# Kernel tuning notes

Hardware: AMD Instinct MI355X
Metric: run time of the kernel (lower is better)

Reference implementation:

```python
import jax, jax.numpy as jnp
import numpy as np


def _interp_ac(x, out_hw):
    """Bilinear resize with align_corners=True; x: (B, C, H, W)."""
    def axis_interp(x, out, axis):
        n = x.shape[axis]
        pos = jnp.linspace(0.0, float(n - 1), out, dtype=x.dtype)
        i0 = jnp.floor(pos).astype(jnp.int32)
        i1 = jnp.minimum(i0 + 1, n - 1)
        w = pos - i0.astype(x.dtype)
        shp = [1] * x.ndim
        shp[axis] = out
        w = w.reshape(shp)
        return jnp.take(x, i0, axis=axis) * (1.0 - w) + jnp.take(x, i1, axis=axis) * w
    x = axis_interp(x, out_hw[0], 2)
    x = axis_interp(x, out_hw[1], 3)
    return x


def _bn(x, gamma, beta, mean, var):
    # eval-mode BatchNorm2d, eps=1e-5; x: (B, C, H, W)
    inv = jax.lax.rsqrt(var + 1e-5)
    return (x - mean[None, :, None, None]) * (gamma * inv)[None, :, None, None] + beta[None, :, None, None]


def setup_inputs() -> dict:
    key = jax.random.key(0)
    ks = jax.random.split(key, 4)
    B, C_low, H_low, W_low = 8, 64, 256, 256
    C_high, H_high, W_high = 128, 64, 64
    rdm = 64
    return {
        "x_low": jax.random.normal(ks[0], (B, C_low, H_low, W_low), jnp.float32),
        "x_high": jax.random.normal(ks[1], (B, C_high, H_high, W_high), jnp.float32),
        "red_w": jax.random.normal(ks[2], (rdm, C_high), jnp.float32) * 0.05,
        "red_gamma": jnp.ones((rdm,), jnp.float32),
        "red_beta": jnp.zeros((rdm,), jnp.float32),
        "red_mean": jnp.zeros((rdm,), jnp.float32),
        "red_var": jnp.ones((rdm,), jnp.float32),
        "cconv_w": jax.random.normal(ks[3], (rdm, 2 * rdm), jnp.float32) * 0.05,
        "cconv_b": jnp.zeros((rdm,), jnp.float32),
        "cc_gamma": jnp.ones((rdm,), jnp.float32),
        "cc_beta": jnp.zeros((rdm,), jnp.float32),
        "cc_mean": jnp.zeros((rdm,), jnp.float32),
        "cc_var": jnp.ones((rdm,), jnp.float32),
    }


def reference(x_low, x_high, red_w, red_gamma, red_beta, red_mean, red_var,
              cconv_w, cconv_b, cc_gamma, cc_beta, cc_mean, cc_var):
    B, Cl, Hl, Wl = x_low.shape
    _, Ch, Hh, Wh = x_high.shape
    N = Hh * Wh
    xh_sg = jax.lax.stop_gradient(x_high)  # torch uses x_high.detach() everywhere

    # --- cosine channel-attention branch ---
    xl = _interp_ac(x_low, (Hh, Wh)).reshape(B, Cl, N)   # (B, Cl, N)
    xh = xh_sg.reshape(B, Ch, N)                          # (B, Ch, N)
    nl = jnp.sqrt(jnp.sum(xl * xl, axis=2, keepdims=True)) + 1e-12  # (B, Cl, 1)
    nh = jnp.sqrt(jnp.sum(xh * xh, axis=2, keepdims=True)) + 1e-12  # (B, Ch, 1)
    cos = jnp.einsum('bcn,bdn->bcd', xl / nl, xh / nh)    # (B, Cl, Ch)
    cos = jax.nn.softmax(cos, axis=2)
    x_high_cos = jnp.einsum('bcd,bdn->bcn', cos, xh).reshape(B, Cl, Hh, Wh)
    x_high_cos = _interp_ac(x_high_cos, (Hl, Wl))         # (B, Cl, Hl, Wl)

    # --- reduced high-level branch (1x1 conv + BN + ReLU) ---
    red = jnp.einsum('oc,bchw->bohw', red_w, xh_sg)
    red = jax.nn.relu(_bn(red, red_gamma, red_beta, red_mean, red_var))
    red = _interp_ac(red, (Hl, Wl))                       # (B, rdm, Hl, Wl)

    # --- channel gate: adaptive avg pool -> 1x1 conv -> BN -> sigmoid ---
    pooled = jnp.mean(jnp.concatenate([x_low, red], axis=1), axis=(2, 3))  # (B, 2*rdm)
    att = pooled @ cconv_w.T + cconv_b                    # (B, rdm)
    att = jax.nn.sigmoid(_bn(att[:, :, None, None], cc_gamma, cc_beta, cc_mean, cc_var))
    red = red * att

    # --- sigmoid diffs + ReLU ---
    sl = jax.nn.sigmoid(x_low)
    diff = jnp.concatenate([sl - jax.nn.sigmoid(x_high_cos),
                            sl - jax.nn.sigmoid(red)], axis=1)
    return jax.nn.relu(diff)
```

## Files before the change

### kernel.cpp

```cpp
#include <hip/hip_runtime.h>
#include <math.h>

#define NPIX 4096
#define NLOW 65536
#define NRSTAGE 19

__device__ __forceinline__ float sigmoidf_(float x){
  return __builtin_amdgcn_rcpf(1.0f + __expf(-x));
}

__device__ __forceinline__ float wave_sum(float v){
  #pragma unroll
  for(int o=32;o;o>>=1) v += __shfl_down(v, o, 64);
  return v;
}

__global__ __launch_bounds__(512) void k_down(const float* __restrict__ xlow,
    float* __restrict__ xl, float* __restrict__ ssql, float* __restrict__ sum_low){
  __shared__ float rows[17*256];
  __shared__ float sd[16];
  int bc = blockIdx.x;
  const float4* X4 = (const float4*)(xlow + (size_t)bc*NLOW);
  float4* R4 = (float4*)rows;
  const float D = 255.0f/63.0f;
  float sum = 0.f, ssq = 0.f;
  int rt = threadIdx.x >> 6, j = threadIdx.x & 63;

  for(int it=0; it<16; ++it){
    int base = 16*it;
    __syncthreads();
    for(int i=threadIdx.x; i<1024; i+=512){
      float4 v = X4[base*64 + i];
      R4[i] = v;
      sum += (v.x+v.y)+(v.z+v.w);
    }
    if(threadIdx.x < 64){
      int srow = base+16; if(srow > 255) srow = 255;
      R4[1024 + threadIdx.x] = X4[srow*64 + threadIdx.x];
    }
    __syncthreads();
    int i0 = (int)ceilf((float)base / D);
    int i = i0 + rt;
    if(i < 64){
      float ph = i*D; int h0 = (int)ph; if(h0 > 255) h0 = 255;
      if((h0 >> 4) == it){
        float fh = ph - (float)h0;
        int h1 = h0+1; if(h1 > 255) h1 = 255;
        int hl = h0 - base, hl2 = h1 - base;
        float pw = j*D; int w0 = (int)pw; if(w0 > 255) w0 = 255;
        float fw = pw - (float)w0;
        int w1 = w0+1; if(w1 > 255) w1 = 255;
        const float* r0 = rows + hl*256; const float* r1 = rows + hl2*256;
        float v = (1.f-fh)*((1.f-fw)*r0[w0] + fw*r0[w1])
                +      fh *((1.f-fw)*r1[w0] + fw*r1[w1]);
        xl[(size_t)bc*NPIX + i*64 + j] = v;
        ssq += v*v;
      }
    }
  }
  float wa = wave_sum(sum), wb = wave_sum(ssq);
  int w = threadIdx.x >> 6;
  if((threadIdx.x & 63) == 0){ sd[w] = wa; sd[8+w] = wb; }
  __syncthreads();
  if(threadIdx.x == 0){
    float a = 0.f, b2 = 0.f;
    #pragma unroll
    for(int k=0;k<8;k++){ a += sd[k]; b2 += sd[8+k]; }
    sum_low[bc] = a;
    ssql[bc]    = b2;
  }
}

__global__ __launch_bounds__(256) void k_ssqh(const float* __restrict__ xh, float* __restrict__ ssqh){
  __shared__ float sd[4];
  int bd = blockIdx.x;
  const float4* P = (const float4*)(xh + (size_t)bd*NPIX);
  float s = 0.f;
  for(int i=threadIdx.x; i<NPIX/4; i+=256){
    float4 v = P[i];
    s += v.x*v.x + v.y*v.y + v.z*v.z + v.w*v.w;
  }
  float w = wave_sum(s);
  if((threadIdx.x & 63) == 0) sd[threadIdx.x >> 6] = w;
  __syncthreads();
  if(threadIdx.x == 0) ssqh[bd] = sd[0]+sd[1]+sd[2]+sd[3];
}

__global__ __launch_bounds__(256) void k_cospart(const float* __restrict__ xl,
                                                 const float* __restrict__ xh,
                                                 float* __restrict__ cospart){
  __shared__ float xls[64*65];
  __shared__ float xhs[128*65];
  int b = blockIdx.x >> 6;
  int chk = blockIdx.x & 63;
  int n0 = chk * 64;
  for(int idx = threadIdx.x; idx < 64*64; idx += 256){
    int c = idx >> 6, k = idx & 63;
    xls[c*65 + k] = xl[((size_t)b*64 + c)*NPIX + n0 + k];
  }
  for(int idx = threadIdx.x; idx < 128*64; idx += 256){
    int d = idx >> 6, k = idx & 63;
    xhs[d*65 + k] = xh[((size_t)b*128 + d)*NPIX + n0 + k];
  }
  __syncthreads();
  int ci = threadIdx.x & 15, di = threadIdx.x >> 4;
  int c0 = ci*4, d0 = di*8;
  float acc[4][8];
  #pragma unroll
  for(int i=0;i<4;i++)
    #pragma unroll
    for(int j=0;j<8;j++) acc[i][j] = 0.f;
  for(int k=0;k<64;k++){
    float a0 = xls[(c0+0)*65 + k];
    float a1 = xls[(c0+1)*65 + k];
    float a2 = xls[(c0+2)*65 + k];
    float a3 = xls[(c0+3)*65 + k];
    #pragma unroll
    for(int j=0;j<8;j++){
      float bv = xhs[(d0+j)*65 + k];
      acc[0][j] += a0*bv; acc[1][j] += a1*bv; acc[2][j] += a2*bv; acc[3][j] += a3*bv;
    }
  }
  float* op = cospart + (size_t)(b*64 + chk)*8192;
  #pragma unroll
  for(int i=0;i<4;i++){
    float4 v0 = make_float4(acc[i][0],acc[i][1],acc[i][2],acc[i][3]);
    float4 v1 = make_float4(acc[i][4],acc[i][5],acc[i][6],acc[i][7]);
    float4* dst = (float4*)(op + (c0+i)*128 + d0);
    dst[0] = v0; dst[1] = v1;
  }
}

__global__ __launch_bounds__(128) void k_softmax(const float* __restrict__ cospart,
    const float* __restrict__ ssql, const float* __restrict__ ssqh, float* __restrict__ p){
  int b = blockIdx.x >> 6, c = blockIdx.x & 63;
  int d = threadIdx.x;
  float s = 0.f;
  for(int chk=0; chk<64; chk++)
    s += cospart[(size_t)(b*64 + chk)*8192 + c*128 + d];
  float nl = sqrtf(ssql[b*64 + c]) + 1e-12f;
  float nh = sqrtf(ssqh[b*128 + d]) + 1e-12f;
  float cosv = s / (nl * nh);
  __shared__ float sm[2], ssum[2];
  float m = cosv;
  #pragma unroll
  for(int o=32;o;o>>=1) m = fmaxf(m, __shfl_xor(m, o, 64));
  if((threadIdx.x & 63) == 0) sm[threadIdx.x >> 6] = m;
  __syncthreads();
  m = fmaxf(sm[0], sm[1]);
  float e = __expf(cosv - m);
  float t = e;
  #pragma unroll
  for(int o=32;o;o>>=1) t += __shfl_xor(t, o, 64);
  if((threadIdx.x & 63) == 0) ssum[threadIdx.x >> 6] = t;
  __syncthreads();
  t = ssum[0] + ssum[1];
  p[(size_t)(b*64 + c)*128 + d] = e * __builtin_amdgcn_rcpf(t);
}

__global__ __launch_bounds__(256) void k_pv(const float* __restrict__ p, const float* __restrict__ red_w,
    const float* __restrict__ xh,
    const float* __restrict__ rg, const float* __restrict__ rb,
    const float* __restrict__ rm, const float* __restrict__ rv,
    float* __restrict__ xhc, float* __restrict__ red64){
  __shared__ float P_s[128*65];
  int b = blockIdx.x >> 6, chk = blockIdx.x & 63;
  int n0 = chk * 64;
  int ni = threadIdx.x & 7, ri = threadIdx.x >> 3;
  int r0 = 4*ri;
  float acc[4][8];
  #pragma unroll
  for(int i=0;i<4;i++)
    #pragma unroll
    for(int j=0;j<8;j++) acc[i][j] = 0.f;
  const float* xrow = xh + (size_t)b*128*NPIX + n0 + 8*ni;
  for(int half=0; half<2; ++half){
    int kb = half*64;
    __syncthreads();
    for(int idx = threadIdx.x; idx < 128*64; idx += 256){
      int r = idx >> 6, kk = idx & 63;
      int k = kb + kk;
      P_s[r*65 + kk] = (r < 64) ? p[((size_t)b*64 + r)*128 + k]
                                : red_w[(size_t)(r-64)*128 + k];
    }
    __syncthreads();
    #pragma unroll 4
    for(int kk=0; kk<64; ++kk){
      int k = kb + kk;
      float4 x0 = *(const float4*)(xrow + (size_t)k*NPIX);
      float4 x1 = *(const float4*)(xrow + (size_t)k*NPIX + 4);
      #pragma unroll
      for(int rr=0; rr<4; rr++){
        float pw = P_s[(r0+rr)*65 + kk];
        acc[rr][0] += pw*x0.x; acc[rr][1] += pw*x0.y; acc[rr][2] += pw*x0.z; acc[rr][3] += pw*x0.w;
        acc[rr][4] += pw*x1.x; acc[rr][5] += pw*x1.y; acc[rr][6] += pw*x1.z; acc[rr][7] += pw*x1.w;
      }
    }
  }
  #pragma unroll
  for(int rr=0; rr<4; rr++){
    int r = r0 + rr;
    if(r < 64){
      float* dst = xhc + ((size_t)b*64 + r)*NPIX + n0 + 8*ni;
      *(float4*)dst     = make_float4(acc[rr][0],acc[rr][1],acc[rr][2],acc[rr][3]);
      *(float4*)(dst+4) = make_float4(acc[rr][4],acc[rr][5],acc[rr][6],acc[rr][7]);
    } else {
      int o = r - 64;
      float sc = rg[o] * rsqrtf(rv[o] + 1e-5f);
      float bs = rb[o] - rm[o]*sc;
      float* dst = red64 + ((size_t)b*64 + o)*NPIX + n0 + 8*ni;
      *(float4*)dst     = make_float4(fmaxf(fmaf(acc[rr][0],sc,bs),0.f), fmaxf(fmaf(acc[rr][1],sc,bs),0.f),
                                      fmaxf(fmaf(acc[rr][2],sc,bs),0.f), fmaxf(fmaf(acc[rr][3],sc,bs),0.f));
      *(float4*)(dst+4) = make_float4(fmaxf(fmaf(acc[rr][4],sc,bs),0.f), fmaxf(fmaf(acc[rr][5],sc,bs),0.f),
                                      fmaxf(fmaf(acc[rr][6],sc,bs),0.f), fmaxf(fmaf(acc[rr][7],sc,bs),0.f));
    }
  }
}

__global__ __launch_bounds__(256) void k_redmean(const float* __restrict__ red64, float* __restrict__ redmean){
  __shared__ float wv[64];
  __shared__ float sd[4];
  int bo = blockIdx.x;
  if(threadIdx.x < 64){
    int i = threadIdx.x;
    const float U = 63.0f/255.0f;
    float acc = 0.f;
    for(int k=0;k<256;k++){
      float pos = k*U;
      int i0 = (int)pos; if(i0>63) i0=63;
      float f = pos - (float)i0;
      int i1 = i0+1; if(i1>63) i1=63;
      if(i0==i) acc += 1.0f - f;
      if(i1==i) acc += f;
    }
    wv[i] = acc;
  }
  __syncthreads();
  const float* R = red64 + (size_t)bo*NPIX;
  float acc = 0.f;
  for(int t=threadIdx.x; t<NPIX; t+=256){
    int i = t>>6, j = t&63;
    acc += wv[i]*wv[j]*R[t];
  }
  float w = wave_sum(acc);
  if((threadIdx.x & 63) == 0) sd[threadIdx.x >> 6] = w;
  __syncthreads();
  if(threadIdx.x == 0) redmean[bo] = (sd[0]+sd[1]+sd[2]+sd[3]) * (1.0f/65536.0f);
}

__global__ __launch_bounds__(256) void k_final(const float* __restrict__ xlow,
    const float* __restrict__ xhc, const float* __restrict__ red64,
    const float* __restrict__ sum_low, const float* __restrict__ redmean,
    const float* __restrict__ cw, const float* __restrict__ cb,
    const float* __restrict__ g, const float* __restrict__ be,
    const float* __restrict__ mu, const float* __restrict__ va,
    float* __restrict__ out){
  __shared__ float sx[NRSTAGE*64];
  __shared__ float sr[NRSTAGE*64];
  __shared__ float s_red[2];
  __shared__ float s_att;
  int bc = blockIdx.x >> 2;
  int sl_ = blockIdx.x & 3;
  int b = bc >> 6, c = bc & 63;
  int h_start = sl_ * 64;
  const float U = 63.0f/255.0f;
  int r_lo = (int)(h_start*U);
  {
    const float* Ax = xhc   + (size_t)bc*NPIX;
    const float* Ar = red64 + (size_t)bc*NPIX;
    for(int i=threadIdx.x; i<NRSTAGE*16; i+=256){
      int row = i>>4, c4 = i&15;
      int srow = r_lo + row; if(srow > 63) srow = 63;
      ((float4*)sx)[i] = *(const float4*)(Ax + srow*64 + c4*4);
      ((float4*)sr)[i] = *(const float4*)(Ar + srow*64 + c4*4);
    }
  }
  if(threadIdx.x < 128){
    int j = threadIdx.x;
    float pj = (j < 64) ? sum_low[b*64 + j]*(1.0f/65536.0f) : redmean[b*64 + (j-64)];
    float t = cw[c*128 + j] * pj;
    float w = wave_sum(t);
    if((j & 63) == 0) s_red[j >> 6] = w;
  }
  __syncthreads();
  if(threadIdx.x == 0){
    float acc = s_red[0] + s_red[1] + cb[c];
    float sc = g[c] * rsqrtf(va[c] + 1e-5f);
    s_att = sigmoidf_((acc - mu[c])*sc + be[c]);
  }
  __syncthreads();
  float a = s_att;

  int ct = threadIdx.x & 63;
  int rt = threadIdx.x >> 6;
  float fw_[4]; bool dw_[4];
  int c0;
  {
    float pw0 = (4*ct)*U; c0 = (int)pw0; if(c0 > 63) c0 = 63;
    #pragma unroll
    for(int i=0;i<4;i++){
      int w = 4*ct + i;
      float pw = w*U;
      int w0 = (int)pw; if(w0 > 63) w0 = 63;
      fw_[i] = pw - (float)w0;
      dw_[i] = (w0 > c0);
    }
  }
  const float* XL = xlow + (size_t)bc*NLOW;
  float* O1 = out + ((size_t)(b*128) + c)*NLOW;
  float* O2 = O1 + (size_t)64*NLOW;

  #pragma unroll
  for(int it=0; it<4; ++it){
    int hbase = h_start + (it*4 + rt)*4;
    int r0 = (int)(hbase*U);
    float ax[3][3], ar[3][3];
    #pragma unroll
    for(int rr=0; rr<3; rr++){
      int rcl = r0 + rr; if(rcl > 63) rcl = 63;
      int rb_ = (rcl - r_lo)*64;
      #pragma unroll
      for(int cc=0; cc<3; cc++){
        int ccl = c0 + cc; if(ccl > 63) ccl = 63;
        ax[rr][cc] = sx[rb_ + ccl];
        ar[rr][cc] = sr[rb_ + ccl];
      }
    }
    float tx[3][4], tr_[3][4];
    #pragma unroll
    for(int rr=0; rr<3; rr++){
      #pragma unroll
      for(int i=0;i<4;i++){
        float lx0 = dw_[i] ? ax[rr][1] : ax[rr][0];
        float lx1 = dw_[i] ? ax[rr][2] : ax[rr][1];
        tx[rr][i] = lx0 + fw_[i]*(lx1 - lx0);
        float lr0 = dw_[i] ? ar[rr][1] : ar[rr][0];
        float lr1 = dw_[i] ? ar[rr][2] : ar[rr][1];
        tr_[rr][i] = lr0 + fw_[i]*(lr1 - lr0);
      }
    }
    #pragma unroll
    for(int hh=0; hh<4; ++hh){
      int h = hbase + hh;
      float ph = h*U;
      int h0 = (int)ph; if(h0 > 63) h0 = 63;
      float fh = ph - (float)h0;
      bool e = (h0 > r0);
      float4 xv = *(const float4*)(XL + h*256 + ct*4);
      float xvv[4] = {xv.x, xv.y, xv.z, xv.w};
      float o1[4], o2[4];
      #pragma unroll
      for(int i=0;i<4;i++){
        float ax0 = e ? tx[1][i] : tx[0][i];
        float ax1 = e ? tx[2][i] : tx[1][i];
        float vx = ax0 + fh*(ax1 - ax0);
        float ar0 = e ? tr_[1][i] : tr_[0][i];
        float ar1 = e ? tr_[2][i] : tr_[1][i];
        float vr = ar0 + fh*(ar1 - ar0);
        float sl = sigmoidf_(xvv[i]);
        o1[i] = fmaxf(sl - sigmoidf_(vx), 0.f);
        o2[i] = fmaxf(sl - sigmoidf_(vr*a), 0.f);
      }
      *(float4*)(O1 + h*256 + ct*4) = make_float4(o1[0],o1[1],o1[2],o1[3]);
      *(float4*)(O2 + h*256 + ct*4) = make_float4(o2[0],o2[1],o2[2],o2[3]);
    }
  }
}

extern "C" void kernel_launch(void* const* d_in, const int* in_sizes, int n_in,
                              void* d_out, int out_size, void* d_ws, size_t ws_size,
                              hipStream_t stream) {
  const float* x_low   = (const float*)d_in[0];
  const float* x_high  = (const float*)d_in[1];
  const float* red_w   = (const float*)d_in[2];
  const float* red_g   = (const float*)d_in[3];
  const float* red_b   = (const float*)d_in[4];
  const float* red_m   = (const float*)d_in[5];
  const float* red_v   = (const float*)d_in[6];
  const float* cconv_w = (const float*)d_in[7];
  const float* cconv_b = (const float*)d_in[8];
  const float* cc_g    = (const float*)d_in[9];
  const float* cc_b    = (const float*)d_in[10];
  const float* cc_m    = (const float*)d_in[11];
  const float* cc_v    = (const float*)d_in[12];
  float* out = (float*)d_out;
  float* ws  = (float*)d_ws;

  float* bufA    = ws;
  float* bufB    = ws + 2097152;
  float* p       = ws + 6291456;
  float* sum_low = ws + 6356992;
  float* ssql    = ws + 6357504;
  float* ssqh    = ws + 6358016;
  float* redmean = ws + 6359040;

  hipLaunchKernelGGL(k_down,    dim3(512),  dim3(512), 0, stream, x_low, bufA, ssql, sum_low);
  hipLaunchKernelGGL(k_ssqh,    dim3(1024), dim3(256), 0, stream, x_high, ssqh);
  hipLaunchKernelGGL(k_cospart, dim3(512),  dim3(256), 0, stream, bufA, x_high, bufB);
  hipLaunchKernelGGL(k_softmax, dim3(512),  dim3(128), 0, stream, bufB, ssql, ssqh, p);
  hipLaunchKernelGGL(k_pv,      dim3(512),  dim3(256), 0, stream, p, red_w, x_high,
                     red_g, red_b, red_m, red_v, bufB, bufA);
  hipLaunchKernelGGL(k_redmean, dim3(512),  dim3(256), 0, stream, bufA, redmean);
  hipLaunchKernelGGL(k_final,   dim3(2048), dim3(256), 0, stream, x_low, bufB, bufA,
                     sum_low, redmean, cconv_w, cconv_b, cc_g, cc_b, cc_m, cc_v, out);
}
```

Baseline: 187.1 us.

## Merge ssqh into downsample kernel, split rows, fold redmean into pv

Merges the x_high sum-of-squares kernel into the downsample kernel as extra blocks, and splits each downsample channel across two blocks to double parallelism, with partial sums combined by consumers. Computes the weighted mean of the reduced branch inside k_pv epilogue via per-chunk partials, removing the separate k_redmean kernel and its re-read of red64. This cuts two launches and one pass over a 2M-float buffer, at the cost of extra partial-sum reads in softmax and k_final.

```diff
diff --git a/kernel.cpp b/kernel.cpp
--- a/kernel.cpp
+++ b/kernel.cpp
@@ -15,18 +15,39 @@
   return v;
 }
 
-__global__ __launch_bounds__(512) void k_down(const float* __restrict__ xlow,
-    float* __restrict__ xl, float* __restrict__ ssql, float* __restrict__ sum_low){
+__global__ __launch_bounds__(512) void k_pre(const float* __restrict__ xlow,
+    const float* __restrict__ xh,
+    float* __restrict__ xl, float* __restrict__ ssql2, float* __restrict__ sum_low2,
+    float* __restrict__ ssqh){
   __shared__ float rows[17*256];
   __shared__ float sd[16];
-  int bc = blockIdx.x;
+  int bid = blockIdx.x;
+  if(bid >= 1024){
+    int s = bid - 1024;
+    int h = threadIdx.x >> 8, tid = threadIdx.x & 255;
+    int bd = 2*s + h;
+    const float4* P = (const float4*)(xh + (size_t)bd*NPIX);
+    float acc = 0.f;
+    #pragma unroll
+    for(int i=tid; i<1024; i+=256){
+      float4 v = P[i];
+      acc += v.x*v.x + v.y*v.y + v.z*v.z + v.w*v.w;
+    }
+    float w = wave_sum(acc);
+    if((threadIdx.x & 63) == 0) sd[threadIdx.x >> 6] = w;
+    __syncthreads();
+    if(tid == 0) ssqh[bd] = sd[h*4+0]+sd[h*4+1]+sd[h*4+2]+sd[h*4+3];
+    return;
+  }
+  int bc = bid >> 1, half = bid & 1;
   const float4* X4 = (const float4*)(xlow + (size_t)bc*NLOW);
   float4* R4 = (float4*)rows;
   const float D = 255.0f/63.0f;
   float sum = 0.f, ssq = 0.f;
   int rt = threadIdx.x >> 6, j = threadIdx.x & 63;
 
-  for(int it=0; it<16; ++it){
+  for(int w=0; w<8; ++w){
+    int it = half*8 + w;
     int base = 16*it;
     __syncthreads();
     for(int i=threadIdx.x; i<1024; i+=512){
@@ -59,31 +80,16 @@
     }
   }
   float wa = wave_sum(sum), wb = wave_sum(ssq);
-  int w = threadIdx.x >> 6;
-  if((threadIdx.x & 63) == 0){ sd[w] = wa; sd[8+w] = wb; }
+  int wi = threadIdx.x >> 6;
+  if((threadIdx.x & 63) == 0){ sd[wi] = wa; sd[8+wi] = wb; }
   __syncthreads();
   if(threadIdx.x == 0){
     float a = 0.f, b2 = 0.f;
     #pragma unroll
     for(int k=0;k<8;k++){ a += sd[k]; b2 += sd[8+k]; }
-    sum_low[bc] = a;
-    ssql[bc]    = b2;
-  }
-}
-
-__global__ __launch_bounds__(256) void k_ssqh(const float* __restrict__ xh, float* __restrict__ ssqh){
-  __shared__ float sd[4];
-  int bd = blockIdx.x;
-  const float4* P = (const float4*)(xh + (size_t)bd*NPIX);
-  float s = 0.f;
-  for(int i=threadIdx.x; i<NPIX/4; i+=256){
-    float4 v = P[i];
-    s += v.x*v.x + v.y*v.y + v.z*v.z + v.w*v.w;
-  }
-  float w = wave_sum(s);
-  if((threadIdx.x & 63) == 0) sd[threadIdx.x >> 6] = w;
-  __syncthreads();
-  if(threadIdx.x == 0) ssqh[bd] = sd[0]+sd[1]+sd[2]+sd[3];
+    sum_low2[bc*2 + half] = a;
+    ssql2[bc*2 + half]    = b2;
+  }
 }
 
 __global__ __launch_bounds__(256) void k_cospart(const float* __restrict__ xl,
@@ -132,13 +138,13 @@
 }
 
 __global__ __launch_bounds__(128) void k_softmax(const float* __restrict__ cospart,
-    const float* __restrict__ ssql, const float* __restrict__ ssqh, float* __restrict__ p){
+    const float* __restrict__ ssql2, const float* __restrict__ ssqh, float* __restrict__ p){
   int b = blockIdx.x >> 6, c = blockIdx.x & 63;
   int d = threadIdx.x;
   float s = 0.f;
   for(int chk=0; chk<64; chk++)
     s += cospart[(size_t)(b*64 + chk)*8192 + c*128 + d];
-  float nl = sqrtf(ssql[b*64 + c]) + 1e-12f;
+  float nl = sqrtf(ssql2[(b*64 + c)*2] + ssql2[(b*64 + c)*2 + 1]) + 1e-12f;
   float nh = sqrtf(ssqh[b*128 + d]) + 1e-12f;
   float cosv = s / (nl * nh);
   __shared__ float sm[2], ssum[2];
@@ -162,65 +168,13 @@
     const float* __restrict__ xh,
     const float* __restrict__ rg, const float* __restrict__ rb,
     const float* __restrict__ rm, const float* __restrict__ rv,
-    float* __restrict__ xhc, float* __restrict__ red64){
+    float* __restrict__ xhc, float* __restrict__ red64, float* __restrict__ part_buf){
   __shared__ float P_s[128*65];
+  __shared__ float wvv[64];
   int b = blockIdx.x >> 6, chk = blockIdx.x & 63;
   int n0 = chk * 64;
   int ni = threadIdx.x & 7, ri = threadIdx.x >> 3;
   int r0 = 4*ri;
-  float acc[4][8];
-  #pragma unroll
-  for(int i=0;i<4;i++)
-    #pragma unroll
-    for(int j=0;j<8;j++) acc[i][j] = 0.f;
-  const float* xrow = xh + (size_t)b*128*NPIX + n0 + 8*ni;
-  for(int half=0; half<2; ++half){
-    int kb = half*64;
-    __syncthreads();
-    for(int idx = threadIdx.x; idx < 128*64; idx += 256){
-      int r = idx >> 6, kk = idx & 63;
-      int k = kb + kk;
-      P_s[r*65 + kk] = (r < 64) ? p[((size_t)b*64 + r)*128 + k]
-                                : red_w[(size_t)(r-64)*128 + k];
-    }
-    __syncthreads();
-    #pragma unroll 4
-    for(int kk=0; kk<64; ++kk){
-      int k = kb + kk;
-      float4 x0 = *(const float4*)(xrow + (size_t)k*NPIX);
-      float4 x1 = *(const float4*)(xrow + (size_t)k*NPIX + 4);
-      #pragma unroll
-      for(int rr=0; rr<4; rr++){
-        float pw = P_s[(r0+rr)*65 + kk];
-        acc[rr][0] += pw*x0.x; acc[rr][1] += pw*x0.y; acc[rr][2] += pw*x0.z; acc[rr][3] += pw*x0.w;
-        acc[rr][4] += pw*x1.x; acc[rr][5] += pw*x1.y; acc[rr][6] += pw*x1.z; acc[rr][7] += pw*x1.w;
-      }
-    }
-  }
-  #pragma unroll
-  for(int rr=0; rr<4; rr++){
-    int r = r0 + rr;
-    if(r < 64){
-      float* dst = xhc + ((size_t)b*64 + r)*NPIX + n0 + 8*ni;
-      *(float4*)dst     = make_float4(acc[rr][0],acc[rr][1],acc[rr][2],acc[rr][3]);
-      *(float4*)(dst+4) = make_float4(acc[rr][4],acc[rr][5],acc[rr][6],acc[rr][7]);
-    } else {
-      int o = r - 64;
-      float sc = rg[o] * rsqrtf(rv[o] + 1e-5f);
-      float bs = rb[o] - rm[o]*sc;
-      float* dst = red64 + ((size_t)b*64 + o)*NPIX + n0 + 8*ni;
-      *(float4*)dst     = make_float4(fmaxf(fmaf(acc[rr][0],sc,bs),0.f), fmaxf(fmaf(acc[rr][1],sc,bs),0.f),
-                                      fmaxf(fmaf(acc[rr][2],sc,bs),0.f), fmaxf(fmaf(acc[rr][3],sc,bs),0.f));
-      *(float4*)(dst+4) = make_float4(fmaxf(fmaf(acc[rr][4],sc,bs),0.f), fmaxf(fmaf(acc[rr][5],sc,bs),0.f),
-                                      fmaxf(fmaf(acc[rr][6],sc,bs),0.f), fmaxf(fmaf(acc[rr][7],sc,bs),0.f));
-    }
-  }
-}
-
-__global__ __launch_bounds__(256) void k_redmean(const float* __restrict__ red64, float* __restrict__ redmean){
-  __shared__ float wv[64];
-  __shared__ float sd[4];
-  int bo = blockIdx.x;
   if(threadIdx.x < 64){
     int i = threadIdx.x;
     const float U = 63.0f/255.0f;
@@ -233,24 +187,74 @@
       if(i0==i) acc += 1.0f - f;
       if(i1==i) acc += f;
     }
-    wv[i] = acc;
-  }
-  __syncthreads();
-  const float* R = red64 + (size_t)bo*NPIX;
-  float acc = 0.f;
-  for(int t=threadIdx.x; t<NPIX; t+=256){
-    int i = t>>6, j = t&63;
-    acc += wv[i]*wv[j]*R[t];
-  }
-  float w = wave_sum(acc);
-  if((threadIdx.x & 63) == 0) sd[threadIdx.x >> 6] = w;
-  __syncthreads();
-  if(threadIdx.x == 0) redmean[bo] = (sd[0]+sd[1]+sd[2]+sd[3]) * (1.0f/65536.0f);
+    wvv[i] = acc;
+  }
+  float acc[4][8];
+  #pragma unroll
+  for(int i=0;i<4;i++)
+    #pragma unroll
+    for(int j=0;j<8;j++) acc[i][j] = 0.f;
+  const float* xrow = xh + (size_t)b*128*NPIX + n0 + 8*ni;
+  for(int half=0; half<2; ++half){
+    int kb = half*64;
+    __syncthreads();
+    for(int idx = threadIdx.x; idx < 128*64; idx += 256){
+      int r = idx >> 6, kk = idx & 63;
+      int k = kb + kk;
+      P_s[r*65 + kk] = (r < 64) ? p[((size_t)b*64 + r)*128 + k]
+                                : red_w[(size_t)(r-64)*128 + k];
+    }
+    __syncthreads();
+    #pragma unroll 4
+    for(int kk=0; kk<64; ++kk){
+      int k = kb + kk;
+      float4 x0 = *(const float4*)(xrow + (size_t)k*NPIX);
+      float4 x1 = *(const float4*)(xrow + (size_t)k*NPIX + 4);
+      #pragma unroll
+      for(int rr=0; rr<4; rr++){
+        float pw = P_s[(r0+rr)*65 + kk];
+        acc[rr][0] += pw*x0.x; acc[rr][1] += pw*x0.y; acc[rr][2] += pw*x0.z; acc[rr][3] += pw*x0.w;
+        acc[rr][4] += pw*x1.x; acc[rr][5] += pw*x1.y; acc[rr][6] += pw*x1.z; acc[rr][7] += pw*x1.w;
+      }
+    }
+  }
+  if(r0 < 64){
+    #pragma unroll
+    for(int rr=0; rr<4; rr++){
+      int r = r0 + rr;
+      float* dst = xhc + ((size_t)b*64 + r)*NPIX + n0 + 8*ni;
+      *(float4*)dst     = make_float4(acc[rr][0],acc[rr][1],acc[rr][2],acc[rr][3]);
+      *(float4*)(dst+4) = make_float4(acc[rr][4],acc[rr][5],acc[rr][6],acc[rr][7]);
+    }
+  } else {
+    float wj[8];
+    #pragma unroll
+    for(int jj=0;jj<8;jj++) wj[jj] = wvv[8*ni + jj];
+    float wchk = wvv[chk];
+    #pragma unroll
+    for(int rr=0; rr<4; rr++){
+      int o = r0 + rr - 64;
+      float sc = rg[o] * rsqrtf(rv[o] + 1e-5f);
+      float bs = rb[o] - rm[o]*sc;
+      float v[8];
+      #pragma unroll
+      for(int jj=0;jj<8;jj++) v[jj] = fmaxf(fmaf(acc[rr][jj],sc,bs),0.f);
+      float* dst = red64 + ((size_t)b*64 + o)*NPIX + n0 + 8*ni;
+      *(float4*)dst     = make_float4(v[0],v[1],v[2],v[3]);
+      *(float4*)(dst+4) = make_float4(v[4],v[5],v[6],v[7]);
+      float part = 0.f;
+      #pragma unroll
+      for(int jj=0;jj<8;jj++) part += wj[jj]*v[jj];
+      #pragma unroll
+      for(int off=1; off<8; off<<=1) part += __shfl_xor(part, off, 64);
+      if(ni == 0) part_buf[((size_t)b*64 + o)*64 + chk] = wchk * part;
+    }
+  }
 }
 
 __global__ __launch_bounds__(256) void k_final(const float* __restrict__ xlow,
     const float* __restrict__ xhc, const float* __restrict__ red64,
-    const float* __restrict__ sum_low, const float* __restrict__ redmean,
+    const float* __restrict__ sum_low2, const float* __restrict__ part_buf,
     const float* __restrict__ cw, const float* __restrict__ cb,
     const float* __restrict__ g, const float* __restrict__ be,
     const float* __restrict__ mu, const float* __restrict__ va,
@@ -277,7 +281,16 @@
   }
   if(threadIdx.x < 128){
     int j = threadIdx.x;
-    float pj = (j < 64) ? sum_low[b*64 + j]*(1.0f/65536.0f) : redmean[b*64 + (j-64)];
+    float pj;
+    if(j < 64){
+      pj = (sum_low2[(b*64 + j)*2] + sum_low2[(b*64 + j)*2 + 1]) * (1.0f/65536.0f);
+    } else {
+      const float4* pr = (const float4*)(part_buf + ((size_t)b*64 + (j-64))*64);
+      float s4 = 0.f;
+      #pragma unroll
+      for(int q=0;q<16;q++){ float4 v = pr[q]; s4 += (v.x+v.y)+(v.z+v.w); }
+      pj = s4 * (1.0f/65536.0f);
+    }
     float t = cw[c*128 + j] * pj;
     float w = wave_sum(t);
     if((j & 63) == 0) s_red[j >> 6] = w;
@@ -386,21 +399,20 @@
   float* out = (float*)d_out;
   float* ws  = (float*)d_ws;
 
-  float* bufA    = ws;
-  float* bufB    = ws + 2097152;
-  float* p       = ws + 6291456;
-  float* sum_low = ws + 6356992;
-  float* ssql    = ws + 6357504;
-  float* ssqh    = ws + 6358016;
-  float* redmean = ws + 6359040;
-
-  hipLaunchKernelGGL(k_down,    dim3(512),  dim3(512), 0, stream, x_low, bufA, ssql, sum_low);
-  hipLaunchKernelGGL(k_ssqh,    dim3(1024), dim3(256), 0, stream, x_high, ssqh);
+  float* bufA     = ws;
+  float* bufB     = ws + 2097152;
+  float* p        = ws + 6291456;
+  float* sum_low2 = ws + 6356992;
+  float* ssql2    = ws + 6358016;
+  float* ssqh     = ws + 6359040;
+  float* part_buf = ws + 6360064;
+
+  hipLaunchKernelGGL(k_pre,     dim3(1536), dim3(512), 0, stream, x_low, x_high,
+                     bufA, ssql2, sum_low2, ssqh);
   hipLaunchKernelGGL(k_cospart, dim3(512),  dim3(256), 0, stream, bufA, x_high, bufB);
-  hipLaunchKernelGGL(k_softmax, dim3(512),  dim3(128), 0, stream, bufB, ssql, ssqh, p);
+  hipLaunchKernelGGL(k_softmax, dim3(512),  dim3(128), 0, stream, bufB, ssql2, ssqh, p);
   hipLaunchKernelGGL(k_pv,      dim3(512),  dim3(256), 0, stream, p, red_w, x_high,
-                     red_g, red_b, red_m, red_v, bufB, bufA);
-  hipLaunchKernelGGL(k_redmean, dim3(512),  dim3(256), 0, stream, bufA, redmean);
+                     red_g, red_b, red_m, red_v, bufB, bufA, part_buf);
   hipLaunchKernelGGL(k_final,   dim3(2048), dim3(256), 0, stream, x_low, bufB, bufA,
-                     sum_low, redmean, cconv_w, cconv_b, cc_g, cc_b, cc_m, cc_v, out);
-}
+                     sum_low2, part_buf, cconv_w, cconv_b, cc_g, cc_b, cc_m, cc_v, out);
+}
```

New measurement: 172.5 us. -7.8%, faster.
